# Optimization experiments

Hardware: AMD Instinct MI355X
Metric: run time of the kernel (lower is better)

Reference implementation:

```python
import jax, jax.numpy as jnp
import numpy as np

B, C, HEADS, W, Hh = 8, 512, 8, 32, 32
D = C // HEADS  # 64 per-head dim
N = W * Hh      # 1024 spatial tokens


def setup_inputs() -> dict:
    key = jax.random.key(0)
    ks = jax.random.split(key, 10)
    s = 1.0 / np.sqrt(C)
    return {
        "x": jax.random.normal(ks[0], (B, C, W, Hh), dtype=jnp.float32),
        "Wq": jax.random.normal(ks[1], (C, C), dtype=jnp.float32) * s,
        "bq": jax.random.normal(ks[2], (C,), dtype=jnp.float32) * 0.01,
        "Wk": jax.random.normal(ks[3], (C, C), dtype=jnp.float32) * s,
        "bk": jax.random.normal(ks[4], (C,), dtype=jnp.float32) * 0.01,
        "Wv": jax.random.normal(ks[5], (C, C), dtype=jnp.float32) * s,
        "bv": jax.random.normal(ks[6], (C,), dtype=jnp.float32) * 0.01,
        "rel_h": jax.random.normal(ks[7], (1, HEADS, D, 1, Hh), dtype=jnp.float32),
        "rel_w": jax.random.normal(ks[8], (1, HEADS, D, W, 1), dtype=jnp.float32),
    }


def reference(x, Wq, bq, Wk, bk, Wv, bv, rel_h, rel_w):
    b = x.shape[0]
    xf = x.reshape(b, C, N)  # [B, C, N] — 1x1 conv == per-position linear
    proj = lambda Wm, bm: (jnp.einsum('oc,bcn->bon', Wm, xf) + bm[None, :, None]).reshape(b, HEADS, D, N)
    q = proj(Wq, bq)  # [B, H, D, N]
    k = proj(Wk, bk)
    v = proj(Wv, bv)
    # content-content: q^T k -> [B, H, N, N]
    cc = jnp.einsum('bhdn,bhdm->bhnm', q, k)
    # relative position bias: (rel_h + rel_w) -> [H, D, N], then rel^T @ q
    rel = (rel_h + rel_w).reshape(HEADS, D, N)
    cp = jnp.einsum('hdn,bhdm->bhnm', rel, q)  # [B, H, N, N]
    attn = jax.nn.softmax(cc + cp, axis=-1)
    # out = v @ attn^T : out[d,m] = sum_n v[d,n] * attn[m,n]
    out = jnp.einsum('bhdn,bhmn->bhdm', v, attn)  # [B, H, D, N]
    return out.reshape(b, C, W, Hh)
```

## Files before the change

### kernel.cpp

```cpp
#include <hip/hip_runtime.h>

typedef _Float16 half8 __attribute__((ext_vector_type(8)));
typedef _Float16 half4 __attribute__((ext_vector_type(4)));
typedef __fp16 fp16x2 __attribute__((ext_vector_type(2)));
typedef float f32x4 __attribute__((ext_vector_type(4)));

__device__ __forceinline__ void glds16(const void* g, void* l) {
    __builtin_amdgcn_global_load_lds(
        (const __attribute__((address_space(1))) unsigned int*)g,
        (__attribute__((address_space(3))) unsigned int*)l, 16, 0, 0);
}

__device__ __forceinline__ void swap32(unsigned int& a, unsigned int& b) {
    asm volatile("v_permlane32_swap_b32 %0, %1" : "+v"(a), "+v"(b));
}
__device__ __forceinline__ void swap16(unsigned int& a, unsigned int& b) {
    asm volatile("v_permlane16_swap_b32 %0, %1" : "+v"(a), "+v"(b));
}


__global__ void k_prep_wrel(const float* __restrict__ Wq, const float* __restrict__ Wk,
                            const float* __restrict__ Wv, const float* __restrict__ bq,
                            const float* __restrict__ bk, const float* __restrict__ bv,
                            const float* __restrict__ rel_h, const float* __restrict__ rel_w,
                            _Float16* __restrict__ Wf, float* __restrict__ bias2,
                            _Float16* __restrict__ rel2) {
    int bid = blockIdx.x;
    if (bid < 384) {
        int t = bid * 256 + threadIdx.x;
        int m = t >> 6;
        int c8 = (t & 63) << 3;
        const float* src = (m < 512) ? (Wq + m * 512)
                         : (m < 1024 ? (Wk + (m - 512) * 512) : (Wv + (m - 1024) * 512));
        float4 v0 = *(const float4*)(src + c8);
        float4 v1 = *(const float4*)(src + c8 + 4);
        half8 o;
        o[0] = (_Float16)v0.x; o[1] = (_Float16)v0.y; o[2] = (_Float16)v0.z; o[3] = (_Float16)v0.w;
        o[4] = (_Float16)v1.x; o[5] = (_Float16)v1.y; o[6] = (_Float16)v1.z; o[7] = (_Float16)v1.w;
        *(half8*)(Wf + (size_t)m * 512 + c8) = o;
        if (t < 1536)
            bias2[t] = (t < 512) ? bq[t] : (t < 1024 ? bk[t - 512] : bv[t - 1024]);
    } else {
        int tid = (bid - 384) * 256 + threadIdx.x;
        int h = tid >> 13;
        int rem = tid & 8191;
        int n = rem >> 3;
        int g = rem & 7;
        int hh = n & 31, ww = n >> 5;
        half8 o;
#pragma unroll
        for (int j = 0; j < 8; ++j) {
            int d = g * 8 + j;
            o[j] = (_Float16)(rel_h[(h * 64 + d) * 32 + hh] + rel_w[(h * 64 + d) * 32 + ww]);
        }
        *(half8*)(rel2 + ((size_t)h * 1024 + n) * 64 + g * 8) = o;
    }
}

__global__ __launch_bounds__(256, 3) void k_projb(const _Float16* __restrict__ Wf,
                                                  const float* __restrict__ x,
                                                  const float* __restrict__ bias2,
                                                  _Float16* __restrict__ q2,
                                                  _Float16* __restrict__ k2,
                                                  _Float16* __restrict__ vb) {
    __shared__ __align__(16) _Float16 As[8192];
    __shared__ __align__(16) _Float16 Bs[8192];
    int t = threadIdx.x;
    int lane = t & 63, w = t >> 6;
    int lm = lane & 15, lq = lane >> 4;
    int wr = (w >> 1) * 64, wc = (w & 1) * 64;
    int mb = blockIdx.y * 128, nbase = blockIdx.x * 128, b = blockIdx.z;
    int rl = lane >> 2;
    int csw = ((lane & 3) ^ ((lane >> 3) & 3)) * 8;
    const _Float16* Ag0 = Wf + (size_t)(mb + w * 32 + rl) * 512 + csw;
    const _Float16* Ag1 = Ag0 + 16 * 512;
    int nq = t & 31;
    int ch = t >> 5;
    int bkh = ch >> 2;
    int g2 = ch & 3;
    const float* xb = x + (size_t)b * 512 * 1024 + nbase + nq * 4;
    f32x4 acc[4][4];
#pragma unroll
    for (int i = 0; i < 4; ++i)
#pragma unroll
        for (int j = 0; j < 4; ++j) acc[i][j] = {0.f, 0.f, 0.f, 0.f};
    int fsw = (lq ^ ((lm >> 1) & 3)) * 8;
    for (int k0 = 0; k0 < 512; k0 += 64) {
#pragma unroll
        for (int kh = 0; kh < 2; ++kh) {
            int ko = k0 + kh * 32;
            glds16(Ag0 + ko, &As[kh * 4096 + (w * 32) * 32]);
            glds16(Ag1 + ko, &As[kh * 4096 + (w * 32 + 16) * 32]);
        }
        {
            const float* xp = xb + (size_t)(k0 + ch * 8) * 1024;
            float4 xf0 = *(const float4*)(xp);
            float4 xf1 = *(const float4*)(xp + 1024);
            float4 xf2 = *(const float4*)(xp + 2048);
            float4 xf3 = *(const float4*)(xp + 3072);
            float4 xf4 = *(const float4*)(xp + 4096);
            float4 xf5 = *(const float4*)(xp + 5120);
            float4 xf6 = *(const float4*)(xp + 6144);
            float4 xf7 = *(const float4*)(xp + 7168);
            _Float16* bsh = &Bs[bkh * 4096];
#define STAGE_ROW(j, c0, c1, c2, c3, c4, c5, c6, c7)                     \
            {                                                            \
                int r = nq * 4 + j;                                      \
                int gd = g2 ^ ((r >> 1) & 3);                            \
                half8 h;                                                 \
                h[0] = (_Float16)c0; h[1] = (_Float16)c1;                \
                h[2] = (_Float16)c2; h[3] = (_Float16)c3;                \
                h[4] = (_Float16)c4; h[5] = (_Float16)c5;                \
                h[6] = (_Float16)c6; h[7] = (_Float16)c7;                \
                *(half8*)&bsh[r * 32 + gd * 8] = h;                      \
            }
            STAGE_ROW(0, xf0.x, xf1.x, xf2.x, xf3.x, xf4.x, xf5.x, xf6.x, xf7.x)
            STAGE_ROW(1, xf0.y, xf1.y, xf2.y, xf3.y, xf4.y, xf5.y, xf6.y, xf7.y)
            STAGE_ROW(2, xf0.z, xf1.z, xf2.z, xf3.z, xf4.z, xf5.z, xf6.z, xf7.z)
            STAGE_ROW(3, xf0.w, xf1.w, xf2.w, xf3.w, xf4.w, xf5.w, xf6.w, xf7.w)
#undef STAGE_ROW
        }
        __syncthreads();
#pragma unroll
        for (int kh = 0; kh < 2; ++kh) {
            half8 af[4], bfr[4];
#pragma unroll
            for (int mt = 0; mt < 4; ++mt)
                af[mt] = *(half8*)&As[kh * 4096 + (wr + mt * 16 + lm) * 32 + fsw];
#pragma unroll
            for (int nt = 0; nt < 4; ++nt)
                bfr[nt] = *(half8*)&Bs[kh * 4096 + (wc + nt * 16 + lm) * 32 + fsw];
#pragma unroll
            for (int mt = 0; mt < 4; ++mt)
#pragma unroll
                for (int nt = 0; nt < 4; ++nt)
                    acc[mt][nt] = __builtin_amdgcn_mfma_f32_16x16x32_f16(af[mt], bfr[nt], acc[mt][nt], 0, 0, 0);
        }
        __syncthreads();
    }
    int sect = mb >> 9;
    int hloc = ((mb & 511) + wr) >> 6;
    size_t bh = (size_t)b * 8 + hloc;
    if (sect < 2) {
        float sc = (sect == 0) ? 1.44269504089f : 1.0f;
        _Float16* dst = (sect == 0 ? q2 : k2) + bh * 1024 * 64;
#pragma unroll
        for (int mt = 0; mt < 4; ++mt) {
            int d0 = mt * 16 + lq * 4;
            float bi0 = bias2[mb + wr + d0];
            float bi1 = bias2[mb + wr + d0 + 1];
            float bi2 = bias2[mb + wr + d0 + 2];
            float bi3 = bias2[mb + wr + d0 + 3];
#pragma unroll
            for (int nt = 0; nt < 4; ++nt) {
                int n = nbase + wc + nt * 16 + lm;
                half4 o;
                o[0] = (_Float16)((acc[mt][nt][0] + bi0) * sc);
                o[1] = (_Float16)((acc[mt][nt][1] + bi1) * sc);
                o[2] = (_Float16)((acc[mt][nt][2] + bi2) * sc);
                o[3] = (_Float16)((acc[mt][nt][3] + bi3) * sc);
                *(half4*)(dst + (size_t)n * 64 + d0) = o;
            }
        }
    } else {
        _Float16* dst = vb + bh * 64 * 1024;
#pragma unroll
        for (int mt = 0; mt < 4; ++mt)
#pragma unroll
            for (int reg = 0; reg < 4; ++reg) {
                int d = mt * 16 + lq * 4 + reg;
                float bi = bias2[mb + wr + d];
#pragma unroll
                for (int nt = 0; nt < 4; ++nt) {
                    int n = nbase + wc + nt * 16 + lm;
                    dst[(size_t)d * 1024 + n] = (_Float16)(acc[mt][nt][reg] + bi);
                }
            }
    }
}

__global__ __launch_bounds__(256, 3) void k_attn(const _Float16* __restrict__ q2,
                                                 const _Float16* __restrict__ k2,
                                                 const _Float16* __restrict__ rel2,
                                                 const _Float16* __restrict__ vb,
                                                 float* __restrict__ out) {
    __shared__ __align__(16) char pool[26624];
    _Float16* kb_s = (_Float16*)pool;
    _Float16* v_s  = (_Float16*)(pool + 17408);
    int t = threadIdx.x;
    int lane = t & 63, w = t >> 6;
    int lm = lane & 15, lq = lane >> 4;
    int lin = blockIdx.x;
    int mt0 = lin >> 6;
    int bh_ = lin & 63;
    int h = bh_ & 7, b = bh_ >> 3;
    size_t bh = (size_t)b * 8 + h;
    const _Float16* q2b = q2 + bh * 1024 * 64;
    const _Float16* k2b = k2 + bh * 1024 * 64;
    const _Float16* relb = rel2 + (size_t)h * 1024 * 64;
    const _Float16* vbb = vb + bh * 64 * 1024;
    float* outb = out + bh * 64 * 1024 + mt0 * 128;

    int r = t >> 2, part = t & 3;
    const _Float16* ksrc = ((part < 2) ? (k2b + part * 32) : (q2b + (part - 2) * 32));
    int vc = (t & 3) * 16;
    const _Float16* vsrcb = vbb + (size_t)r * 1024 + vc;
    _Float16* kdst = kb_s + r * 136 + part * 32;
    _Float16* vdst = v_s + r * 72 + vc;

    uint4 kc0, kc1, kc2, kc3, vv0, vv1;
    {
        const uint4* s_ = (const uint4*)(ksrc + (size_t)r * 64);
        kc0 = s_[0]; kc1 = s_[1]; kc2 = s_[2]; kc3 = s_[3];
        const uint4* v_ = (const uint4*)vsrcb;
        vv0 = v_[0]; vv1 = v_[1];
    }

    {
        int n = mt0 * 128 + r;
        const _Float16* src = (part < 2) ? (q2b + (size_t)n * 64 + part * 32)
                                         : (relb + (size_t)n * 64 + (part - 2) * 32);
        ((uint4*)kdst)[0] = ((const uint4*)src)[0];
        ((uint4*)kdst)[1] = ((const uint4*)src)[1];
        ((uint4*)kdst)[2] = ((const uint4*)src)[2];
        ((uint4*)kdst)[3] = ((const uint4*)src)[3];
    }
    __syncthreads();
    half8 ah0[4], ah1[4];
#pragma unroll
    for (int kk = 0; kk < 4; ++kk)
        ah0[kk] = *(half8*)&kb_s[(w * 16 + lm) * 136 + kk * 32 + lq * 8];
    __syncthreads();
    {
        int n = mt0 * 128 + 64 + r;
        const _Float16* src = (part < 2) ? (q2b + (size_t)n * 64 + part * 32)
                                         : (relb + (size_t)n * 64 + (part - 2) * 32);
        ((uint4*)kdst)[0] = ((const uint4*)src)[0];
        ((uint4*)kdst)[1] = ((const uint4*)src)[1];
        ((uint4*)kdst)[2] = ((const uint4*)src)[2];
        ((uint4*)kdst)[3] = ((const uint4*)src)[3];
    }
    __syncthreads();
#pragma unroll
    for (int kk = 0; kk < 4; ++kk)
        ah1[kk] = *(half8*)&kb_s[(w * 16 + lm) * 136 + kk * 32 + lq * 8];
    __syncthreads();

    f32x4 acco0[4], acco1[4];
#pragma unroll
    for (int i = 0; i < 4; ++i) { acco0[i] = {0.f, 0.f, 0.f, 0.f}; acco1[i] = {0.f, 0.f, 0.f, 0.f}; }
    float mrun0 = -3e38f, lrun0 = 0.f, mrun1 = -3e38f, lrun1 = 0.f;

    for (int kt = 0; kt < 16; ++kt) {
        ((uint4*)kdst)[0] = kc0;
        ((uint4*)kdst)[1] = kc1;
        ((uint4*)kdst)[2] = kc2;
        ((uint4*)kdst)[3] = kc3;
        ((uint4*)vdst)[0] = vv0;
        ((uint4*)vdst)[1] = vv1;
        __syncthreads();
        int nn = ((kt + 1) & 15) * 64;
        const uint4* s_ = (const uint4*)(ksrc + (size_t)(nn + r) * 64);
        uint4 kn0 = s_[0], kn1 = s_[1], kn2 = s_[2], kn3 = s_[3];
        const uint4* v_ = (const uint4*)(vsrcb + nn);
        uint4 vn0 = v_[0], vn1 = v_[1];
        f32x4 s0[4], s1[4];
#pragma unroll
        for (int ct = 0; ct < 4; ++ct) { s0[ct] = {0.f, 0.f, 0.f, 0.f}; s1[ct] = {0.f, 0.f, 0.f, 0.f}; }
#pragma unroll
        for (int ct = 0; ct < 4; ++ct) {
            half8 kf[4];
#pragma unroll
            for (int kk = 0; kk < 4; ++kk)
                kf[kk] = *(half8*)&kb_s[(ct * 16 + lm) * 136 + kk * 32 + lq * 8];
#pragma unroll
            for (int kk = 0; kk < 4; ++kk) {
                s0[ct] = __builtin_amdgcn_mfma_f32_16x16x32_f16(kf[kk], ah0[kk], s0[ct], 0, 0, 0);
                s1[ct] = __builtin_amdgcn_mfma_f32_16x16x32_f16(kf[kk], ah1[kk], s1[ct], 0, 0, 0);
            }
        }
        unsigned int pk0[4][2], pk1[4][2];
        {
            float mx = -3e38f;
#pragma unroll
            for (int ct = 0; ct < 4; ++ct)
#pragma unroll
                for (int reg = 0; reg < 4; ++reg) mx = fmaxf(mx, s0[ct][reg]);
            mx = fmaxf(mx, __shfl_xor(mx, 16));
            mx = fmaxf(mx, __shfl_xor(mx, 32));
            float mnew = fmaxf(mrun0, mx);
            float al_ = exp2f(mrun0 - mnew);
            float rs = 0.f;
#pragma unroll
            for (int ct = 0; ct < 4; ++ct) {
                float p0 = exp2f(s0[ct][0] - mnew);
                float p1 = exp2f(s0[ct][1] - mnew);
                float p2 = exp2f(s0[ct][2] - mnew);
                float p3 = exp2f(s0[ct][3] - mnew);
                rs += (p0 + p1) + (p2 + p3);
                pk0[ct][0] = __builtin_bit_cast(unsigned int, __builtin_amdgcn_cvt_pkrtz(p0, p1));
                pk0[ct][1] = __builtin_bit_cast(unsigned int, __builtin_amdgcn_cvt_pkrtz(p2, p3));
            }
            rs += __shfl_xor(rs, 16);
            rs += __shfl_xor(rs, 32);
            lrun0 = lrun0 * al_ + rs;
            mrun0 = mnew;
#pragma unroll
            for (int dt = 0; dt < 4; ++dt) {
                acco0[dt][0] *= al_; acco0[dt][1] *= al_;
                acco0[dt][2] *= al_; acco0[dt][3] *= al_;
            }
        }
        {
            float mx = -3e38f;
#pragma unroll
            for (int ct = 0; ct < 4; ++ct)
#pragma unroll
                for (int reg = 0; reg < 4; ++reg) mx = fmaxf(mx, s1[ct][reg]);
            mx = fmaxf(mx, __shfl_xor(mx, 16));
            mx = fmaxf(mx, __shfl_xor(mx, 32));
            float mnew = fmaxf(mrun1, mx);
            float al_ = exp2f(mrun1 - mnew);
            float rs = 0.f;
#pragma unroll
            for (int ct = 0; ct < 4; ++ct) {
                float p0 = exp2f(s1[ct][0] - mnew);
                float p1 = exp2f(s1[ct][1] - mnew);
                float p2 = exp2f(s1[ct][2] - mnew);
                float p3 = exp2f(s1[ct][3] - mnew);
                rs += (p0 + p1) + (p2 + p3);
                pk1[ct][0] = __builtin_bit_cast(unsigned int, __builtin_amdgcn_cvt_pkrtz(p0, p1));
                pk1[ct][1] = __builtin_bit_cast(unsigned int, __builtin_amdgcn_cvt_pkrtz(p2, p3));
            }
            rs += __shfl_xor(rs, 16);
            rs += __shfl_xor(rs, 32);
            lrun1 = lrun1 * al_ + rs;
            mrun1 = mnew;
#pragma unroll
            for (int dt = 0; dt < 4; ++dt) {
                acco1[dt][0] *= al_; acco1[dt][1] *= al_;
                acco1[dt][2] *= al_; acco1[dt][3] *= al_;
            }
        }
        swap32(pk0[0][0], pk0[1][0]); swap32(pk0[0][1], pk0[1][1]);
        swap32(pk0[2][0], pk0[3][0]); swap32(pk0[2][1], pk0[3][1]);
        swap16(pk0[0][0], pk0[1][0]); swap16(pk0[0][1], pk0[1][1]);
        swap16(pk0[2][0], pk0[3][0]); swap16(pk0[2][1], pk0[3][1]);
        swap32(pk1[0][0], pk1[1][0]); swap32(pk1[0][1], pk1[1][1]);
        swap32(pk1[2][0], pk1[3][0]); swap32(pk1[2][1], pk1[3][1]);
        swap16(pk1[0][0], pk1[1][0]); swap16(pk1[0][1], pk1[1][1]);
        swap16(pk1[2][0], pk1[3][0]); swap16(pk1[2][1], pk1[3][1]);
        half8 p0f[2], p1f[2];
        {
            unsigned int* u;
            u = (unsigned int*)&p0f[0]; u[0] = pk0[0][0]; u[1] = pk0[0][1]; u[2] = pk0[1][0]; u[3] = pk0[1][1];
            u = (unsigned int*)&p0f[1]; u[0] = pk0[2][0]; u[1] = pk0[2][1]; u[2] = pk0[3][0]; u[3] = pk0[3][1];
            u = (unsigned int*)&p1f[0]; u[0] = pk1[0][0]; u[1] = pk1[0][1]; u[2] = pk1[1][0]; u[3] = pk1[1][1];
            u = (unsigned int*)&p1f[1]; u[0] = pk1[2][0]; u[1] = pk1[2][1]; u[2] = pk1[3][0]; u[3] = pk1[3][1];
        }
#pragma unroll
        for (int dt = 0; dt < 4; ++dt) {
            half8 vf0 = *(half8*)&v_s[(dt * 16 + lm) * 72 + lq * 8];
            half8 vf1 = *(half8*)&v_s[(dt * 16 + lm) * 72 + 32 + lq * 8];
            acco0[dt] = __builtin_amdgcn_mfma_f32_16x16x32_f16(vf0, p0f[0], acco0[dt], 0, 0, 0);
            acco0[dt] = __builtin_amdgcn_mfma_f32_16x16x32_f16(vf1, p0f[1], acco0[dt], 0, 0, 0);
            acco1[dt] = __builtin_amdgcn_mfma_f32_16x16x32_f16(vf0, p1f[0], acco1[dt], 0, 0, 0);
            acco1[dt] = __builtin_amdgcn_mfma_f32_16x16x32_f16(vf1, p1f[1], acco1[dt], 0, 0, 0);
        }
        __syncthreads();
        kc0 = kn0; kc1 = kn1; kc2 = kn2; kc3 = kn3;
        vv0 = vn0; vv1 = vn1;
    }
    float li0 = 1.f / lrun0, li1 = 1.f / lrun1;
#pragma unroll
    for (int dt = 0; dt < 4; ++dt)
#pragma unroll
        for (int reg = 0; reg < 4; ++reg) {
            int d = dt * 16 + lq * 4 + reg;
            outb[(size_t)d * 1024 + w * 16 + lm] = acco0[dt][reg] * li0;
            outb[(size_t)d * 1024 + 64 + w * 16 + lm] = acco1[dt][reg] * li1;
        }
}

extern "C" void kernel_launch(void* const* d_in, const int* in_sizes, int n_in,
                              void* d_out, int out_size, void* d_ws, size_t ws_size,
                              hipStream_t stream) {
    const float* x     = (const float*)d_in[0];
    const float* Wq    = (const float*)d_in[1];
    const float* bq    = (const float*)d_in[2];
    const float* Wk    = (const float*)d_in[3];
    const float* bk    = (const float*)d_in[4];
    const float* Wv    = (const float*)d_in[5];
    const float* bv    = (const float*)d_in[6];
    const float* rel_h = (const float*)d_in[7];
    const float* rel_w = (const float*)d_in[8];
    char* ws = (char*)d_ws;
    _Float16* Wf   = (_Float16*)(ws);
    float* bias2   = (float*)(ws + 1572864);
    _Float16* q2   = (_Float16*)(ws + 1579008);
    _Float16* k2   = (_Float16*)(ws + 9967616);
    _Float16* vb   = (_Float16*)(ws + 18356224);
    _Float16* rel2 = (_Float16*)(ws + 26744832);
    float* out = (float*)d_out;

    hipLaunchKernelGGL(k_prep_wrel, dim3(640),      dim3(256), 0, stream,
                       Wq, Wk, Wv, bq, bk, bv, rel_h, rel_w, Wf, bias2, rel2);
    hipLaunchKernelGGL(k_projb,     dim3(8, 12, 8), dim3(256), 0, stream, Wf, x, bias2, q2, k2, vb);
    hipLaunchKernelGGL(k_attn,      dim3(512),      dim3(256), 0, stream, q2, k2, rel2, vb, out);
}
```

Measured before the change: 152.2 us.

## Split attention KV range across two blocks and merge partials

The attention kernel now splits the 1024-key range into two halves, launching 1024 blocks instead of 512. Each block writes unnormalized partial outputs plus running max and sum to workspace. A new merge kernel then combines the two partials with log-sum-exp rescaling. Occupancy hint is raised to 4 blocks per CU. The goal is better CU fill (512 blocks on 256 CUs at 3 per CU underused the GPU), paid for with extra partial-buffer traffic and a fourth launch.

```diff
diff --git a/kernel.cpp b/kernel.cpp
--- a/kernel.cpp
+++ b/kernel.cpp
@@ -2,7 +2,6 @@
 
 typedef _Float16 half8 __attribute__((ext_vector_type(8)));
 typedef _Float16 half4 __attribute__((ext_vector_type(4)));
-typedef __fp16 fp16x2 __attribute__((ext_vector_type(2)));
 typedef float f32x4 __attribute__((ext_vector_type(4)));
 
 __device__ __forceinline__ void glds16(const void* g, void* l) {
@@ -179,11 +178,12 @@
     }
 }
 
-__global__ __launch_bounds__(256, 3) void k_attn(const _Float16* __restrict__ q2,
+__global__ __launch_bounds__(256, 4) void k_attn(const _Float16* __restrict__ q2,
                                                  const _Float16* __restrict__ k2,
                                                  const _Float16* __restrict__ rel2,
                                                  const _Float16* __restrict__ vb,
-                                                 float* __restrict__ out) {
+                                                 float* __restrict__ part,
+                                                 float* __restrict__ ml) {
     __shared__ __align__(16) char pool[26624];
     _Float16* kb_s = (_Float16*)pool;
     _Float16* v_s  = (_Float16*)(pool + 17408);
@@ -191,35 +191,36 @@
     int lane = t & 63, w = t >> 6;
     int lm = lane & 15, lq = lane >> 4;
     int lin = blockIdx.x;
-    int mt0 = lin >> 6;
-    int bh_ = lin & 63;
+    int kvh = lin >> 9;
+    int rest = lin & 511;
+    int mt0 = rest >> 6;
+    int bh_ = rest & 63;
     int h = bh_ & 7, b = bh_ >> 3;
     size_t bh = (size_t)b * 8 + h;
     const _Float16* q2b = q2 + bh * 1024 * 64;
     const _Float16* k2b = k2 + bh * 1024 * 64;
     const _Float16* relb = rel2 + (size_t)h * 1024 * 64;
     const _Float16* vbb = vb + bh * 64 * 1024;
-    float* outb = out + bh * 64 * 1024 + mt0 * 128;
-
-    int r = t >> 2, part = t & 3;
-    const _Float16* ksrc = ((part < 2) ? (k2b + part * 32) : (q2b + (part - 2) * 32));
+
+    int r = t >> 2, part_ = t & 3;
+    const _Float16* ksrc = ((part_ < 2) ? (k2b + part_ * 32) : (q2b + (part_ - 2) * 32));
     int vc = (t & 3) * 16;
     const _Float16* vsrcb = vbb + (size_t)r * 1024 + vc;
-    _Float16* kdst = kb_s + r * 136 + part * 32;
+    _Float16* kdst = kb_s + r * 136 + part_ * 32;
     _Float16* vdst = v_s + r * 72 + vc;
 
     uint4 kc0, kc1, kc2, kc3, vv0, vv1;
     {
-        const uint4* s_ = (const uint4*)(ksrc + (size_t)r * 64);
+        const uint4* s_ = (const uint4*)(ksrc + (size_t)(kvh * 512 + r) * 64);
         kc0 = s_[0]; kc1 = s_[1]; kc2 = s_[2]; kc3 = s_[3];
-        const uint4* v_ = (const uint4*)vsrcb;
+        const uint4* v_ = (const uint4*)(vsrcb + kvh * 512);
         vv0 = v_[0]; vv1 = v_[1];
     }
 
     {
         int n = mt0 * 128 + r;
-        const _Float16* src = (part < 2) ? (q2b + (size_t)n * 64 + part * 32)
-                                         : (relb + (size_t)n * 64 + (part - 2) * 32);
+        const _Float16* src = (part_ < 2) ? (q2b + (size_t)n * 64 + part_ * 32)
+                                          : (relb + (size_t)n * 64 + (part_ - 2) * 32);
         ((uint4*)kdst)[0] = ((const uint4*)src)[0];
         ((uint4*)kdst)[1] = ((const uint4*)src)[1];
         ((uint4*)kdst)[2] = ((const uint4*)src)[2];
@@ -233,8 +234,8 @@
     __syncthreads();
     {
         int n = mt0 * 128 + 64 + r;
-        const _Float16* src = (part < 2) ? (q2b + (size_t)n * 64 + part * 32)
-                                         : (relb + (size_t)n * 64 + (part - 2) * 32);
+        const _Float16* src = (part_ < 2) ? (q2b + (size_t)n * 64 + part_ * 32)
+                                          : (relb + (size_t)n * 64 + (part_ - 2) * 32);
         ((uint4*)kdst)[0] = ((const uint4*)src)[0];
         ((uint4*)kdst)[1] = ((const uint4*)src)[1];
         ((uint4*)kdst)[2] = ((const uint4*)src)[2];
@@ -251,7 +252,7 @@
     for (int i = 0; i < 4; ++i) { acco0[i] = {0.f, 0.f, 0.f, 0.f}; acco1[i] = {0.f, 0.f, 0.f, 0.f}; }
     float mrun0 = -3e38f, lrun0 = 0.f, mrun1 = -3e38f, lrun1 = 0.f;
 
-    for (int kt = 0; kt < 16; ++kt) {
+    for (int kt = kvh * 8; kt < kvh * 8 + 8; ++kt) {
         ((uint4*)kdst)[0] = kc0;
         ((uint4*)kdst)[1] = kc1;
         ((uint4*)kdst)[2] = kc2;
@@ -371,15 +372,59 @@
         kc0 = kn0; kc1 = kn1; kc2 = kn2; kc3 = kn3;
         vv0 = vn0; vv1 = vn1;
     }
-    float li0 = 1.f / lrun0, li1 = 1.f / lrun1;
+    float* pacc = part + (size_t)lin * 8192;
 #pragma unroll
     for (int dt = 0; dt < 4; ++dt)
 #pragma unroll
         for (int reg = 0; reg < 4; ++reg) {
             int d = dt * 16 + lq * 4 + reg;
-            outb[(size_t)d * 1024 + w * 16 + lm] = acco0[dt][reg] * li0;
-            outb[(size_t)d * 1024 + 64 + w * 16 + lm] = acco1[dt][reg] * li1;
-        }
+            pacc[d * 128 + w * 16 + lm] = acco0[dt][reg];
+            pacc[d * 128 + 64 + w * 16 + lm] = acco1[dt][reg];
+        }
+    if (lq == 0) {
+        float* mlb = ml + (size_t)lin * 256;
+        float2 v0; v0.x = mrun0; v0.y = lrun0;
+        float2 v1; v1.x = mrun1; v1.y = lrun1;
+        *(float2*)&mlb[(w * 16 + lm) * 2] = v0;
+        *(float2*)&mlb[(64 + w * 16 + lm) * 2] = v1;
+    }
+}
+
+__global__ __launch_bounds__(256) void k_merge(const float* __restrict__ part,
+                                               const float* __restrict__ ml,
+                                               float* __restrict__ out) {
+    __shared__ float s0s[128], s1s[128];
+    int rest = blockIdx.x;
+    int t = threadIdx.x;
+    const float* pa0 = part + (size_t)rest * 8192;
+    const float* pa1 = part + (size_t)(rest + 512) * 8192;
+    if (t < 128) {
+        const float* ml0 = ml + (size_t)rest * 256 + t * 2;
+        const float* ml1 = ml + (size_t)(rest + 512) * 256 + t * 2;
+        float m0 = ml0[0], l0 = ml0[1];
+        float m1 = ml1[0], l1 = ml1[1];
+        float ms = fmaxf(m0, m1);
+        float a0 = exp2f(m0 - ms), a1 = exp2f(m1 - ms);
+        float li = 1.f / (a0 * l0 + a1 * l1);
+        s0s[t] = a0 * li;
+        s1s[t] = a1 * li;
+    }
+    __syncthreads();
+    int bh = rest & 63, mt0 = rest >> 6;
+    float* ob = out + (size_t)bh * 65536 + mt0 * 128;
+    int d = t >> 2, mq = (t & 3) * 32;
+#pragma unroll
+    for (int j = 0; j < 8; ++j) {
+        int m = mq + j * 4;
+        float4 A0 = *(const float4*)&pa0[d * 128 + m];
+        float4 A1 = *(const float4*)&pa1[d * 128 + m];
+        float4 o;
+        o.x = s0s[m] * A0.x + s1s[m] * A1.x;
+        o.y = s0s[m + 1] * A0.y + s1s[m + 1] * A1.y;
+        o.z = s0s[m + 2] * A0.z + s1s[m + 2] * A1.z;
+        o.w = s0s[m + 3] * A0.w + s1s[m + 3] * A1.w;
+        *(float4*)&ob[(size_t)d * 1024 + m] = o;
+    }
 }
 
 extern "C" void kernel_launch(void* const* d_in, const int* in_sizes, int n_in,
@@ -401,10 +446,13 @@
     _Float16* k2   = (_Float16*)(ws + 9967616);
     _Float16* vb   = (_Float16*)(ws + 18356224);
     _Float16* rel2 = (_Float16*)(ws + 26744832);
+    float* part    = (float*)(ws + 27793408);
+    float* ml      = (float*)(ws + 61347840);
     float* out = (float*)d_out;
 
     hipLaunchKernelGGL(k_prep_wrel, dim3(640),      dim3(256), 0, stream,
                        Wq, Wk, Wv, bq, bk, bv, rel_h, rel_w, Wf, bias2, rel2);
     hipLaunchKernelGGL(k_projb,     dim3(8, 12, 8), dim3(256), 0, stream, Wf, x, bias2, q2, k2, vb);
-    hipLaunchKernelGGL(k_attn,      dim3(512),      dim3(256), 0, stream, q2, k2, rel2, vb, out);
-}
+    hipLaunchKernelGGL(k_attn,      dim3(1024),     dim3(256), 0, stream, q2, k2, rel2, vb, part, ml);
+    hipLaunchKernelGGL(k_merge,     dim3(512),      dim3(256), 0, stream, part, ml, out);
+}
```

After: 240.1 us. 57.7% more time.
